# Performance work log

Measured on AMD Instinct MI355X. Metric: run time of the kernel, lower is better.

## Reference

```python
import jax, jax.numpy as jnp
import numpy as np

B, L, D = 2, 2048, 1024
H = 16
C = 128            # chunk_size
N = L // C         # num chunks
SCALE = float(np.sqrt(D))  # softmax_scale = sqrt(d_model)


def setup_inputs() -> dict:
    key = jax.random.key(0)
    ks = jax.random.split(key, 5)
    return {
        "x": jax.random.normal(ks[0], (B, L, D), dtype=jnp.float32),
        "w_qkv": jax.random.normal(ks[1], (D, 3 * D), dtype=jnp.float32) * (1.0 / np.sqrt(D)),
        "b_qkv": jax.random.normal(ks[2], (3 * D,), dtype=jnp.float32) * 0.02,
        "w_o": jax.random.normal(ks[3], (D, D), dtype=jnp.float32) * (1.0 / np.sqrt(D)),
        "b_o": jax.random.normal(ks[4], (D,), dtype=jnp.float32) * 0.02,
    }


def reference(x, w_qkv, b_qkv, w_o, b_o):
    b, l, d = x.shape
    hd = d // H
    qkv = x @ w_qkv + b_qkv                         # (B,L,3D)
    q, k, v = jnp.split(qkv, 3, axis=-1)
    q = q.reshape(b, l, H, hd)
    k = k.reshape(b, l, H, hd)
    v = v.reshape(b, l, H, hd)

    q_chunks = q.reshape(b, N, C, H, hd)
    k_chunks = k.reshape(b, N, C, H, hd)
    # mean_pool over the chunk dim
    q_pool = q_chunks.mean(axis=2)                  # (B,N,H,hd)
    k_pool = k_chunks.mean(axis=2)

    token2chunk = jnp.einsum('blhd,bnhd->bhln', q, k_pool)          # (B,H,L,N)
    chunk2token = jnp.einsum('bnhd,bnchd->bhnc', q_pool, k_chunks)  # (B,H,N,C)
    # outer product over (n,c) -> full (B,H,L,L) score matrix
    A = token2chunk[..., :, None] * chunk2token[:, :, None, :, :]   # (B,H,L,N,C)
    A = A.reshape(b, H, l, l)

    # direct intra-chunk attention overwrites the diagonal blocks
    direct = jnp.einsum('bnqhd,bnkhd->bhnqk', q_chunks, k_chunks)   # (B,H,N,C,C)
    A6 = A.reshape(b, H, N, C, N, C)
    eye = jnp.eye(N, dtype=bool)[:, None, :, None]                  # (N,1,N,1)
    A6 = jnp.where(eye, direct[:, :, :, :, None, :], A6)
    A = A6.reshape(b, H, l, l)

    # causal mask applied multiplicatively (masked scores become 0, NOT -inf)
    causal = jnp.tril(jnp.ones((l, l), dtype=bool))
    A = jnp.where(causal, A, 0.0) / SCALE
    A = jax.nn.softmax(A, axis=-1)

    out = jnp.einsum('bhqv,bvhd->bhqd', A, v)       # (B,H,L,hd)
    out = out.transpose(0, 2, 1, 3).reshape(b, l, d)
    return out @ w_o + b_o
```

## Files before the change

kernel.cpp:

```cpp
#include <hip/hip_runtime.h>
#include <math.h>

#define B_   2
#define L_   2048
#define D_   1024
#define H_   16
#define HD_  64
#define C_   128
#define N_   16
#define INV_SCALE 0.03125f

typedef _Float16 h8 __attribute__((ext_vector_type(8)));
typedef _Float16 h4 __attribute__((ext_vector_type(4)));
typedef float    f4 __attribute__((ext_vector_type(4)));

#define MFMA16(a, b, c) __builtin_amdgcn_mfma_f32_16x16x32_f16((a), (b), (c), 0, 0, 0)

__device__ __forceinline__ void gl_lds16(const void* g, void* l) {
  __builtin_amdgcn_global_load_lds(
      (const __attribute__((address_space(1))) void*)g,
      (__attribute__((address_space(3))) void*)l, 16, 0, 0);
}

__global__ __launch_bounds__(256) void prep_kernel(
    const float* __restrict__ X, _Float16* __restrict__ Xh,
    const float* __restrict__ Wq, _Float16* __restrict__ WqT,
    const float* __restrict__ Wo, _Float16* __restrict__ WoT)
{
  __shared__ float ts[32][36];
  const int tid = threadIdx.x;
  const int id = blockIdx.x;
  if (id < 4096) {
    int i = id * 1024 + tid * 4;
    float4 v = *(const float4*)(X + i);
    h4 o = { (_Float16)v.x, (_Float16)v.y, (_Float16)v.z, (_Float16)v.w };
    *(h4*)(Xh + i) = o;
    return;
  }
  const float* W; _Float16* WT; int Nc, bx, by;
  if (id < 7168) {
    int idx = id - 4096;
    W = Wq; WT = WqT; Nc = 3072; bx = idx % 96; by = idx / 96;
  } else {
    int idx = id - 7168;
    W = Wo; WT = WoT; Nc = 1024; bx = idx & 31; by = idx >> 5;
  }
  const int n0 = bx * 32, k0 = by * 32;
  {
    int kr = tid >> 3, nc4 = (tid & 7) * 4;
    float4 v = *(const float4*)&W[(size_t)(k0 + kr) * Nc + n0 + nc4];
    ts[kr][nc4+0] = v.x; ts[kr][nc4+1] = v.y; ts[kr][nc4+2] = v.z; ts[kr][nc4+3] = v.w;
  }
  __syncthreads();
  {
    int nr = tid >> 3, kc4 = (tid & 7) * 4;
    h4 o = { (_Float16)ts[kc4+0][nr], (_Float16)ts[kc4+1][nr],
             (_Float16)ts[kc4+2][nr], (_Float16)ts[kc4+3][nr] };
    *(h4*)&WT[(size_t)(n0 + nr) * 1024 + k0 + kc4] = o;
  }
}

template<int MT>
__global__ __launch_bounds__(256, 4) void gemm16_kernel(
    const _Float16* __restrict__ A, const _Float16* __restrict__ Bt,
    const float* __restrict__ bias,
    _Float16* __restrict__ Qh, _Float16* __restrict__ Kh, _Float16* __restrict__ VT,
    float* __restrict__ out,
    float* __restrict__ QP, float* __restrict__ KP, float* __restrict__ VCS,
    int Kd, int mode)
{
  constexpr int SM = MT / 32;
  __shared__ __align__(16) _Float16 As[2][MT * 32];
  __shared__ __align__(16) _Float16 Bs[2][4096];
  __shared__ float cred[2][128];
  const int tid = threadIdx.x;
  const int lane = tid & 63, w = tid >> 6;
  const int q = lane >> 4, r = lane & 15;
  const int mb = (w >> 1) * (MT / 2);
  const int nb = (w & 1) * 64;

  int m0, n0;
  {
    const int id = blockIdx.x;
    const int xcd = id & 7, slot = id >> 3;
    if constexpr (MT == 128) {
      n0 = (xcd * 3 + (slot % 3)) * 128;
      m0 = (slot / 3) * 128;
    } else {
      n0 = xcd * 128;
      m0 = slot * 64;
    }
  }

  const int Rr = tid >> 2;
  const int cd = (tid & 3) ^ ((Rr >> 1) & 3);
  const _Float16* Ag = A + (size_t)(m0 + Rr) * Kd + cd * 8;
  const _Float16* Bg = Bt + (size_t)(n0 + Rr) * Kd + cd * 8;
  const size_t rowStep = (size_t)64 * Kd;

  f4 acc[SM][4];
  #pragma unroll
  for (int s = 0; s < SM; ++s)
    #pragma unroll
    for (int t = 0; t < 4; ++t) acc[s][t] = (f4){0.f, 0.f, 0.f, 0.f};

  const int nIter = Kd >> 5;
  const int koff = (q ^ ((r >> 1) & 3)) << 3;

  auto stage = [&](int bf, int kt) {
    _Float16* Asl = &As[bf][w * 512];
    _Float16* Bsl = &Bs[bf][w * 512];
    gl_lds16(Ag + kt, Asl);
    if constexpr (MT == 128) gl_lds16(Ag + kt + rowStep, Asl + 2048);
    gl_lds16(Bg + kt, Bsl);
    gl_lds16(Bg + kt + rowStep, Bsl + 2048);
  };

  stage(0, 0);

  for (int it = 0; it < nIter; ++it) {
    __syncthreads();
    if (it + 1 < nIter) stage((it + 1) & 1, (it + 1) << 5);
    const _Float16* Ab = As[it & 1];
    const _Float16* Bb = Bs[it & 1];
    h8 af[SM], bf4[4];
    #pragma unroll
    for (int s = 0; s < SM; ++s)
      af[s] = *(const h8*)&Ab[(mb + s * 16 + r) * 32 + koff];
    #pragma unroll
    for (int t = 0; t < 4; ++t)
      bf4[t] = *(const h8*)&Bb[(nb + t * 16 + r) * 32 + koff];
    #pragma unroll
    for (int s = 0; s < SM; ++s)
      #pragma unroll
      for (int t = 0; t < 4; ++t)
        acc[s][t] = MFMA16(af[s], bf4[t], acc[s][t]);
  }

  if (mode == 0) {
    #pragma unroll
    for (int t = 0; t < 4; ++t) {
      int gn = n0 + nb + t * 16 + r;
      float bj = bias[gn];
      int which = gn >> 10, rem = gn & 1023;
      int h2 = rem >> 6, d2 = rem & 63;
      if (which < 2) {
        _Float16* dst = which == 0 ? Qh : Kh;
        #pragma unroll
        for (int s = 0; s < SM; ++s)
          #pragma unroll
          for (int i = 0; i < 4; ++i) {
            int gm = m0 + mb + s * 16 + q * 4 + i;
            int b2 = gm >> 11, l2 = gm & 2047;
            dst[(((size_t)(b2 * H_ + h2)) * L_ + l2) * HD_ + d2] =
                (_Float16)(acc[s][t][i] + bj);
          }
      } else {
        #pragma unroll
        for (int s = 0; s < SM; ++s) {
          int gm0 = m0 + mb + s * 16 + q * 4;
          int b2 = gm0 >> 11, l2 = gm0 & 2047;
          h4 hv = { (_Float16)(acc[s][t][0] + bj), (_Float16)(acc[s][t][1] + bj),
                    (_Float16)(acc[s][t][2] + bj), (_Float16)(acc[s][t][3] + bj) };
          *(h4*)&VT[((size_t)(b2 * H_ + h2) * HD_ + d2) * L_ + l2] = hv;
        }
      }
    }
    float colsum[4];
    #pragma unroll
    for (int t = 0; t < 4; ++t) {
      float s2 = 0.f;
      #pragma unroll
      for (int s = 0; s < SM; ++s)
        #pragma unroll
        for (int i = 0; i < 4; ++i) s2 += acc[s][t][i];
      s2 += __shfl_xor(s2, 16);
      s2 += __shfl_xor(s2, 32);
      colsum[t] = s2;
    }
    if (q == 0) {
      #pragma unroll
      for (int t = 0; t < 4; ++t)
        cred[w >> 1][nb + t * 16 + r] = colsum[t];
    }
    __syncthreads();
    if (tid < 128) {
      int jj = tid;
      float ssum = cred[0][jj] + cred[1][jj];
      int gn = n0 + jj;
      float bj = bias[gn];
      int which = gn >> 10, rem = gn & 1023;
      int h2 = rem >> 6, d2 = rem & 63;
      int b2 = m0 >> 11, nch = (m0 & 2047) >> 7;
      size_t o = (((size_t)(b2 * H_ + h2)) * N_ + nch) * HD_ + d2;
      if (which == 0)      QP[o] = ssum * (1.f / 128.f) + bj;
      else if (which == 1) KP[o] = ssum * (1.f / 128.f) + bj;
      else                 VCS[o] = ssum + 128.f * bj;
    }
  } else {
    #pragma unroll
    for (int t = 0; t < 4; ++t) {
      int gn = n0 + nb + t * 16 + r;
      float bj = bias[gn];
      #pragma unroll
      for (int s = 0; s < SM; ++s)
        #pragma unroll
        for (int i = 0; i < 4; ++i) {
          int gm = m0 + mb + s * 16 + q * 4 + i;
          out[(size_t)gm * 1024 + gn] = acc[s][t][i] + bj;
        }
    }
  }
}

__global__ __launch_bounds__(128) void pool2_kernel(
    const float* __restrict__ QP, const _Float16* __restrict__ Kh,
    const float* __restrict__ VCS,
    float* __restrict__ C2T, float* __restrict__ C2TMX, float* __restrict__ C2TMN,
    float* __restrict__ CSUF)
{
  __shared__ float qp_s[64];
  __shared__ float red[4];
  if (blockIdx.x >= 512) {
    int bh = blockIdx.x - 512, d = threadIdx.x;
    if (d < 64) {
      float run = 0.f;
      for (int n = N_ - 1; n >= 0; --n) {
        size_t o = ((size_t)bh * N_ + n) * HD_ + d;
        CSUF[o] = run;
        run += VCS[o];
      }
    }
    return;
  }
  int bh = blockIdx.x >> 4, n = blockIdx.x & 15, tid = threadIdx.x;
  int w = tid >> 6, lane = tid & 63;
  if (tid < 64) qp_s[tid] = QP[((size_t)bh * N_ + n) * HD_ + tid];
  const _Float16* kr = Kh + (((size_t)bh * L_) + n * C_ + tid) * HD_;
  h8 kv[8];
  #pragma unroll
  for (int c8 = 0; c8 < 8; ++c8) kv[c8] = *(const h8*)(kr + c8 * 8);
  __syncthreads();
  float s = 0.f;
  #pragma unroll
  for (int c8 = 0; c8 < 8; ++c8)
    #pragma unroll
    for (int j = 0; j < 8; ++j)
      s = fmaf((float)kv[c8][j], qp_s[c8 * 8 + j], s);
  C2T[((size_t)bh * N_ + n) * C_ + tid] = s;
  float mx = s, mn = s;
  #pragma unroll
  for (int st = 1; st <= 32; st <<= 1) {
    mx = fmaxf(mx, __shfl_xor(mx, st));
    mn = fminf(mn, __shfl_xor(mn, st));
  }
  if (lane == 0) { red[w * 2] = mx; red[w * 2 + 1] = mn; }
  __syncthreads();
  if (tid == 0) {
    C2TMX[bh * N_ + n] = fmaxf(red[0], red[2]);
    C2TMN[bh * N_ + n] = fminf(red[1], red[3]);
  }
}

__global__ __launch_bounds__(512, 4) void attn4_kernel(
    const _Float16* __restrict__ Qh, const _Float16* __restrict__ Kh,
    const _Float16* __restrict__ VT,
    const float* __restrict__ C2T, const float* __restrict__ C2TMX,
    const float* __restrict__ C2TMN, const float* __restrict__ CSUF,
    const float* __restrict__ KP, _Float16* __restrict__ AOh)
{
  __shared__ __align__(16) _Float16 buf0[8192];
  __shared__ __align__(16) _Float16 buf1[8192];
  __shared__ __align__(16) _Float16 buf2[8192];
  __shared__ __align__(16) _Float16 kp_s[1024];
  __shared__ __align__(16) float c2t_s[2][128];

  const int tid = threadIdx.x;
  const int w = tid >> 6, lane = tid & 63;
  const int q = lane >> 4, r = lane & 15;
  const int r7 = r & 7;
  const int id = blockIdx.x;
  const int bh = ((id & 7) << 2) + ((id >> 3) & 3);
  const int nq = 15 - (id >> 5);
  const int l0 = nq * 128;
  const int rowA = l0 + w * 16 + r;
  const int pcw = w * 16 + r;
  const size_t bhL = (size_t)bh * L_;
  const int b2 = bh >> 4, h2 = bh & 15;

  auto stageV = [&](_Float16* buf, int n) {
    #pragma unroll
    for (int j2 = 0; j2 < 2; ++j2) {
      int f = j2 * 512 + tid;
      int d = f >> 4, p = f & 15;
      int c16 = p ^ (d & 7);
      gl_lds16(VT + ((size_t)bh * HD_ + d) * L_ + n * C_ + c16 * 8,
               buf + (size_t)(j2 * 512 + w * 64) * 8);
    }
  };
  auto stageK = [&](_Float16* buf, int n) {
    #pragma unroll
    for (int j2 = 0; j2 < 2; ++j2) {
      int f = j2 * 512 + tid;
      int c = f >> 3, p = f & 7;
      int ck = p ^ (c & 7);
      gl_lds16(Kh + (bhL + n * C_ + c) * HD_ + ck * 8,
               buf + (size_t)(j2 * 512 + w * 64) * 8);
    }
  };
  auto stageC = [&](int bf, int n) {
    if (tid < 32)
      gl_lds16(C2T + ((size_t)bh * N_ + n) * C_ + tid * 4, &c2t_s[bf][0]);
  };

  if (tid < 256) {
    int n4 = tid >> 4, d4 = (tid & 15) * 4;
    float4 kpv = *(const float4*)&KP[((size_t)bh * N_ + n4) * HD_ + d4];
    int sd = ((((d4 >> 3) ^ (n4 & 7)) << 3) | (d4 & 7));
    h4 hv = { (_Float16)kpv.x, (_Float16)kpv.y, (_Float16)kpv.z, (_Float16)kpv.w };
    *(h4*)&kp_s[n4 * 64 + sd] = hv;
  }
  h8 qa0 = *(const h8*)(Qh + (bhL + rowA) * HD_ + q * 8);
  h8 qa1 = *(const h8*)(Qh + (bhL + rowA) * HD_ + 32 + q * 8);
  float mxL = C2TMX[bh * N_ + r];
  float mnL = C2TMN[bh * N_ + r];
  stageK(buf0, nq);
  stageV(buf2, nq);
  if (nq >= 1) stageC(0, nq - 1);
  __syncthreads();

  f4 tvacc = (f4){0.f, 0.f, 0.f, 0.f};
  {
    h8 kpa0 = *(const h8*)&kp_s[r * 64 + ((q ^ r7) << 3)];
    h8 kpa1 = *(const h8*)&kp_s[r * 64 + (((4 + q) ^ r7) << 3)];
    tvacc = MFMA16(kpa0, qa0, tvacc);
    tvacc = MFMA16(kpa1, qa1, tvacc);
  }
  float tvs[4];
  #pragma unroll
  for (int i = 0; i < 4; ++i) tvs[i] = tvacc[i] * INV_SCALE;

  float pm = -1e30f;
  #pragma unroll
  for (int i = 0; i < 4; ++i) {
    int n = q * 4 + i;
    float mx = __shfl(mxL, n);
    float mn = __shfl(mnL, n);
    float cm = fmaxf(tvs[i] * mx, tvs[i] * mn);
    pm = (n < nq) ? fmaxf(pm, cm) : pm;
  }
  pm = fmaxf(pm, __shfl_xor(pm, 16));
  pm = fmaxf(pm, __shfl_xor(pm, 32));

  f4 sc[8];
  #pragma unroll
  for (int u = 0; u < 8; ++u) sc[u] = (f4){0.f, 0.f, 0.f, 0.f};
  #pragma unroll
  for (int u = 0; u < 8; ++u) {
    h8 kb0 = *(const h8*)&buf0[(u * 16 + r) * 64 + ((q ^ r7) << 3)];
    h8 kb1 = *(const h8*)&buf0[(u * 16 + r) * 64 + (((4 + q) ^ r7) << 3)];
    sc[u] = MFMA16(qa0, kb0, sc[u]);
    sc[u] = MFMA16(qa1, kb1, sc[u]);
  }

  float rm[4] = {-1e30f, -1e30f, -1e30f, -1e30f};
  #pragma unroll
  for (int u = 0; u < 8; ++u) {
    int lcol = u * 16 + r;
    #pragma unroll
    for (int i = 0; i < 4; ++i) {
      int lrow = w * 16 + q * 4 + i;
      float v = sc[u][i] * INV_SCALE;
      v = (lcol <= lrow) ? v : -1e30f;
      sc[u][i] = v;
      rm[i] = fmaxf(rm[i], v);
    }
  }
  #pragma unroll
  for (int i = 0; i < 4; ++i) {
    rm[i] = fmaxf(rm[i], __shfl_xor(rm[i], 1));
    rm[i] = fmaxf(rm[i], __shfl_xor(rm[i], 2));
    rm[i] = fmaxf(rm[i], __shfl_xor(rm[i], 4));
    rm[i] = fmaxf(rm[i], __shfl_xor(rm[i], 8));
  }
  const int srcl = (r >> 2) << 4;
  const int ri = r & 3;
  float t0 = __shfl(rm[0], srcl), t1 = __shfl(rm[1], srcl);
  float t2 = __shfl(rm[2], srcl), t3 = __shfl(rm[3], srcl);
  float myrm = ri == 0 ? t0 : ri == 1 ? t1 : ri == 2 ? t2 : t3;

  const float M = fmaxf(fmaxf(pm, myrm), 0.f);
  const float e0 = __expf(-M);
  float Mc[4];
  #pragma unroll
  for (int i = 0; i < 4; ++i) Mc[i] = __shfl(M, (q << 2) + i);

  float cs[4] = {0.f, 0.f, 0.f, 0.f};
  #pragma unroll
  for (int u = 0; u < 8; ++u)
    #pragma unroll
    for (int i = 0; i < 4; ++i) {
      float v = sc[u][i];
      float p = (v > -1e29f) ? __expf(v - Mc[i]) : 0.f;
      sc[u][i] = p;
      cs[i] += p;
    }
  #pragma unroll
  for (int i = 0; i < 4; ++i) {
    cs[i] += __shfl_xor(cs[i], 1);
    cs[i] += __shfl_xor(cs[i], 2);
    cs[i] += __shfl_xor(cs[i], 4);
    cs[i] += __shfl_xor(cs[i], 8);
  }
  float c0 = __shfl(cs[0], srcl), c1 = __shfl(cs[1], srcl);
  float c2 = __shfl(cs[2], srcl), c3 = __shfl(cs[3], srcl);
  float den = ri == 0 ? c0 : ri == 1 ? c1 : ri == 2 ? c2 : c3;

  __syncthreads();

  _Float16* pw = (w < 4) ? (buf0 + w * 2048) : (buf1 + (w - 4) * 2048);
  #pragma unroll
  for (int u = 0; u < 8; ++u)
    #pragma unroll
    for (int i = 0; i < 4; ++i) {
      int row = q * 4 + i, col = u * 16 + r;
      pw[row * 128 + ((((col >> 3) ^ (row & 7)) << 3) | (col & 7))] =
          (_Float16)sc[u][i];
    }

  f4 oacc[4], sacc[4];
  #pragma unroll
  for (int t = 0; t < 4; ++t) {
    oacc[t] = (f4){0.f, 0.f, 0.f, 0.f};
    sacc[t] = (f4){0.f, 0.f, 0.f, 0.f};
  }
  #pragma unroll
  for (int s = 0; s < 4; ++s) {
    h8 pa = *(const h8*)&pw[r * 128 + (((s * 4 + q) ^ r7) << 3)];
    h8 mk;
    #pragma unroll
    for (int j2 = 0; j2 < 8; ++j2)
      mk[j2] = (_Float16)((s * 32 + q * 8 + j2 > pcw) ? 1.f : 0.f);
    #pragma unroll
    for (int t = 0; t < 4; ++t) {
      h8 vb = *(const h8*)&buf2[(t * 16 + r) * 128 + (((s * 4 + q) ^ r7) << 3)];
      oacc[t] = MFMA16(pa, vb, oacc[t]);
      sacc[t] = MFMA16(mk, vb, sacc[t]);
    }
  }

  __syncthreads();
  if (nq >= 1) stageV(buf1, nq - 1);

  for (int n = nq - 1; n >= 0; --n) {
    const int k = nq - 1 - n;
    _Float16* curb = (k & 1) ? buf2 : buf1;
    __syncthreads();
    if (n >= 1) {
      stageV((k & 1) ? buf1 : buf2, n - 1);
      stageC((k + 1) & 1, n - 1);
    }
    int i0 = n & 3;
    float tvx = i0 == 0 ? tvs[0] : i0 == 1 ? tvs[1] : i0 == 2 ? tvs[2] : tvs[3];
    float tvn = __shfl(tvx, ((n >> 2) << 4) + r);
    float csum = 0.f;
    const float* c2p = c2t_s[k & 1];
    #pragma unroll
    for (int s = 0; s < 4; ++s) {
      const float* cp = &c2p[s * 32 + q * 8];
      float4 ca = *(const float4*)cp;
      float4 cb = *(const float4*)(cp + 4);
      float p0 = __expf(tvn * ca.x - M), p1 = __expf(tvn * ca.y - M);
      float p2 = __expf(tvn * ca.z - M), p3 = __expf(tvn * ca.w - M);
      float p4 = __expf(tvn * cb.x - M), p5 = __expf(tvn * cb.y - M);
      float p6 = __expf(tvn * cb.z - M), p7 = __expf(tvn * cb.w - M);
      csum += p0 + p1 + p2 + p3 + p4 + p5 + p6 + p7;
      h8 pa = { (_Float16)p0, (_Float16)p1, (_Float16)p2, (_Float16)p3,
                (_Float16)p4, (_Float16)p5, (_Float16)p6, (_Float16)p7 };
      #pragma unroll
      for (int t = 0; t < 4; ++t) {
        h8 vb = *(const h8*)&curb[(t * 16 + r) * 128 + (((s * 4 + q) ^ r7) << 3)];
        oacc[t] = MFMA16(pa, vb, oacc[t]);
      }
    }
    csum += __shfl_xor(csum, 16);
    csum += __shfl_xor(csum, 32);
    den += csum;
  }

  int cnt = (L_ - 1) - rowA;
  den += e0 * (float)cnt;
  float e0r[4], dnr[4];
  #pragma unroll
  for (int i = 0; i < 4; ++i) {
    e0r[i] = __shfl(e0,  (q << 2) + i);
    dnr[i] = __shfl(den, (q << 2) + i);
  }
  #pragma unroll
  for (int t = 0; t < 4; ++t) {
    int d = t * 16 + r;
    float csf = CSUF[((size_t)bh * N_ + nq) * HD_ + d];
    #pragma unroll
    for (int i = 0; i < 4; ++i) {
      int row = l0 + w * 16 + q * 4 + i;
      float suffix = sacc[t][i] + csf;
      float o = (oacc[t][i] + e0r[i] * suffix) / dnr[i];
      AOh[((size_t)b2 * L_ + row) * D_ + h2 * HD_ + d] = (_Float16)o;
    }
  }
}

extern "C" void kernel_launch(void* const* d_in, const int* in_sizes, int n_in,
                              void* d_out, int out_size, void* d_ws, size_t ws_size,
                              hipStream_t stream)
{
  (void)in_sizes; (void)n_in; (void)out_size; (void)ws_size;
  const float* x     = (const float*)d_in[0];
  const float* w_qkv = (const float*)d_in[1];
  const float* b_qkv = (const float*)d_in[2];
  const float* w_o   = (const float*)d_in[3];
  const float* b_o   = (const float*)d_in[4];
  float* out = (float*)d_out;

  char* p = (char*)d_ws;
  _Float16* xh   = (_Float16*)p; p += (size_t)4194304 * 2;
  _Float16* wqT  = (_Float16*)p; p += (size_t)3145728 * 2;
  _Float16* woT  = (_Float16*)p; p += (size_t)1048576 * 2;
  _Float16* Qh   = (_Float16*)p; p += (size_t)4194304 * 2;
  _Float16* Kh   = (_Float16*)p; p += (size_t)4194304 * 2;
  _Float16* VT   = (_Float16*)p; p += (size_t)4194304 * 2;
  _Float16* AOh  = (_Float16*)p; p += (size_t)4194304 * 2;
  float*    C2T  = (float*)p;    p += (size_t)65536 * 4;
  float*    QP   = (float*)p;    p += (size_t)32768 * 4;
  float*    KP   = (float*)p;    p += (size_t)32768 * 4;
  float*    VCS  = (float*)p;    p += (size_t)32768 * 4;
  float*    CSUF = (float*)p;    p += (size_t)32768 * 4;
  float*    MXa  = (float*)p;    p += (size_t)512 * 4;
  float*    MNa  = (float*)p;    p += (size_t)512 * 4;

  prep_kernel<<<8192, 256, 0, stream>>>(x, xh, w_qkv, wqT, w_o, woT);
  gemm16_kernel<128><<<768, 256, 0, stream>>>(
      xh, wqT, b_qkv, Qh, Kh, VT, nullptr, QP, KP, VCS, D_, 0);
  pool2_kernel<<<544, 128, 0, stream>>>(QP, Kh, VCS, C2T, MXa, MNa, CSUF);
  attn4_kernel<<<512, 512, 0, stream>>>(
      Qh, Kh, VT, C2T, MXa, MNa, CSUF, KP, AOh);
  gemm16_kernel<64><<<512, 256, 0, stream>>>(
      AOh, woT, b_o, nullptr, nullptr, nullptr, out, nullptr, nullptr, nullptr, D_, 1);
}
```

Baseline: 179.5 us.

## Replace QKV GEMM with 256x256-tile pipelined kernel and remap output GEMM blocks

Adds a dedicated QKV projection kernel that uses 256x256 output tiles, 512 threads, double-buffered global-to-LDS loads and explicit waitcnt/sched barriers with setprio around MFMA bursts. It fuses the bias add, head scatter and chunk pooling epilogue the same way the generic kernel did. Larger tiles raise operand reuse and cut global traffic, but the grid shrinks to 192 blocks, fewer than the device's CU count, so some compute units sit idle. The output-projection GEMM also gets a new block-to-XCD mapping that groups M rows per XCD, aiming at better L2 locality.

```diff
diff --git a/kernel.cpp b/kernel.cpp
--- a/kernel.cpp
+++ b/kernel.cpp
@@ -21,6 +21,14 @@
       (const __attribute__((address_space(1))) void*)g,
       (__attribute__((address_space(3))) void*)l, 16, 0, 0);
 }
+
+#define SBAR()  do { __builtin_amdgcn_sched_barrier(0); \
+                     __builtin_amdgcn_s_barrier();      \
+                     __builtin_amdgcn_sched_barrier(0); } while (0)
+#define LGKM0() do { asm volatile("s_waitcnt lgkmcnt(0)" ::: "memory"); \
+                     __builtin_amdgcn_sched_barrier(0); } while (0)
+#define VMW(n)  do { asm volatile("s_waitcnt vmcnt(" #n ")" ::: "memory"); \
+                     __builtin_amdgcn_sched_barrier(0); } while (0)
 
 __global__ __launch_bounds__(256) void prep_kernel(
     const float* __restrict__ X, _Float16* __restrict__ Xh,
@@ -57,6 +65,172 @@
     h4 o = { (_Float16)ts[kc4+0][nr], (_Float16)ts[kc4+1][nr],
              (_Float16)ts[kc4+2][nr], (_Float16)ts[kc4+3][nr] };
     *(h4*)&WT[(size_t)(n0 + nr) * 1024 + k0 + kc4] = o;
+  }
+}
+
+__global__ __launch_bounds__(512, 2) void qkv256_kernel(
+    const _Float16* __restrict__ A, const _Float16* __restrict__ Bt,
+    const float* __restrict__ bias,
+    _Float16* __restrict__ Qh, _Float16* __restrict__ Kh, _Float16* __restrict__ VT,
+    float* __restrict__ QP, float* __restrict__ KP, float* __restrict__ VCS)
+{
+  __shared__ __align__(16) _Float16 As[2][16384];
+  __shared__ __align__(16) _Float16 Bs[2][16384];
+
+  const int tid = threadIdx.x;
+  const int w = tid >> 6, lane = tid & 63;
+  const int q = lane >> 4, r = lane & 15, r7 = r & 7;
+  const int wm = w >> 2, wn = w & 3;
+
+  const int id = blockIdx.x, xcd = id & 7, slot = id >> 3;
+  const int m0 = ((xcd >> 1) * 4 + (slot & 3)) * 256;
+  const int n0 = ((xcd & 1) * 6 + (slot >> 2)) * 256;
+
+  const int srow = tid >> 3;
+  const int spart = (tid & 7) ^ (srow & 7);
+  const _Float16* Asrc = A  + (size_t)(m0 + srow) * 1024 + spart * 8;
+  const _Float16* Bsrc = Bt + (size_t)(n0 + srow) * 1024 + spart * 8;
+  const int ldst = w * 512;
+
+  const int aoffb = (wm * 128 + r) * 64;
+  const int boffb = (wn * 64 + r) * 64;
+  const int k0s = (q ^ r7) << 3;
+  const int k1s = ((4 + q) ^ r7) << 3;
+
+  auto stA = [&](int cc, int ko, int qq) {
+    gl_lds16(Asrc + (size_t)qq * 65536 + ko, &As[cc][qq * 4096 + ldst]);
+  };
+  auto stB = [&](int cc, int ko, int qq) {
+    gl_lds16(Bsrc + (size_t)qq * 65536 + ko, &Bs[cc][qq * 4096 + ldst]);
+  };
+
+  f4 acc[8][4];
+  #pragma unroll
+  for (int m = 0; m < 8; ++m)
+    #pragma unroll
+    for (int n = 0; n < 4; ++n) acc[m][n] = (f4){0.f, 0.f, 0.f, 0.f};
+
+  stB(0, 0, 0); stB(0, 0, 1); stB(0, 0, 2); stB(0, 0, 3);
+  stA(0, 0, 0); stA(0, 0, 2); stA(0, 0, 1); stA(0, 0, 3);
+  VMW(2);
+  SBAR();
+
+  for (int t = 0; t < 16; ++t) {
+    const int c = t & 1;
+    const _Float16* __restrict__ Ab = As[c];
+    const _Float16* __restrict__ Bb = Bs[c];
+    const int kt = (t + 1) << 6;
+    const bool pf = (t < 15);
+    h8 af[4], bf[4];
+
+    #pragma unroll
+    for (int m = 0; m < 4; ++m) af[m] = *(const h8*)&Ab[aoffb + m * 1024 + k0s];
+    #pragma unroll
+    for (int n = 0; n < 4; ++n) bf[n] = *(const h8*)&Bb[boffb + n * 1024 + k0s];
+    if (pf) { stB(c ^ 1, kt, 0); stB(c ^ 1, kt, 1); }
+    SBAR();
+    LGKM0();
+    __builtin_amdgcn_s_setprio(1);
+    #pragma unroll
+    for (int m = 0; m < 4; ++m)
+      #pragma unroll
+      for (int n = 0; n < 4; ++n) acc[m][n] = MFMA16(af[m], bf[n], acc[m][n]);
+    __builtin_amdgcn_s_setprio(0);
+    __builtin_amdgcn_sched_barrier(0);
+    if (pf) { VMW(2); } else { VMW(0); }
+    SBAR();
+
+    #pragma unroll
+    for (int m = 0; m < 4; ++m) af[m] = *(const h8*)&Ab[aoffb + (4 + m) * 1024 + k0s];
+    if (pf) { stB(c ^ 1, kt, 2); stB(c ^ 1, kt, 3); }
+    SBAR();
+    LGKM0();
+    __builtin_amdgcn_s_setprio(1);
+    #pragma unroll
+    for (int m = 0; m < 4; ++m)
+      #pragma unroll
+      for (int n = 0; n < 4; ++n) acc[4 + m][n] = MFMA16(af[m], bf[n], acc[4 + m][n]);
+    __builtin_amdgcn_s_setprio(0);
+    __builtin_amdgcn_sched_barrier(0);
+    SBAR();
+
+    #pragma unroll
+    for (int m = 0; m < 4; ++m) af[m] = *(const h8*)&Ab[aoffb + m * 1024 + k1s];
+    #pragma unroll
+    for (int n = 0; n < 4; ++n) bf[n] = *(const h8*)&Bb[boffb + n * 1024 + k1s];
+    if (pf) { stA(c ^ 1, kt, 0); stA(c ^ 1, kt, 2); }
+    SBAR();
+    LGKM0();
+    __builtin_amdgcn_s_setprio(1);
+    #pragma unroll
+    for (int m = 0; m < 4; ++m)
+      #pragma unroll
+      for (int n = 0; n < 4; ++n) acc[m][n] = MFMA16(af[m], bf[n], acc[m][n]);
+    __builtin_amdgcn_s_setprio(0);
+    __builtin_amdgcn_sched_barrier(0);
+    SBAR();
+
+    #pragma unroll
+    for (int m = 0; m < 4; ++m) af[m] = *(const h8*)&Ab[aoffb + (4 + m) * 1024 + k1s];
+    if (pf) {
+      stA(c ^ 1, kt, 1); stA(c ^ 1, kt, 3);
+      VMW(2);
+    }
+    SBAR();
+    LGKM0();
+    __builtin_amdgcn_s_setprio(1);
+    #pragma unroll
+    for (int m = 0; m < 4; ++m)
+      #pragma unroll
+      for (int n = 0; n < 4; ++n) acc[4 + m][n] = MFMA16(af[m], bf[n], acc[4 + m][n]);
+    __builtin_amdgcn_s_setprio(0);
+    __builtin_amdgcn_sched_barrier(0);
+    SBAR();
+  }
+
+  const int rb = m0 + wm * 128;
+  const int b2 = rb >> 11;
+  const int nch = (rb & 2047) >> 7;
+  #pragma unroll
+  for (int tc = 0; tc < 4; ++tc) {
+    const int gn = n0 + wn * 64 + tc * 16 + r;
+    const float bj = bias[gn];
+    const int which = gn >> 10, rem = gn & 1023;
+    const int h2 = rem >> 6, d2 = rem & 63;
+    if (which < 2) {
+      _Float16* dst = which == 0 ? Qh : Kh;
+      #pragma unroll
+      for (int m = 0; m < 8; ++m)
+        #pragma unroll
+        for (int i = 0; i < 4; ++i) {
+          const int gm = rb + m * 16 + q * 4 + i;
+          const int l2 = gm & 2047;
+          dst[(((size_t)(b2 * H_ + h2)) * L_ + l2) * HD_ + d2] =
+              (_Float16)(acc[m][tc][i] + bj);
+        }
+    } else {
+      #pragma unroll
+      for (int m = 0; m < 8; ++m) {
+        const int gm0 = rb + m * 16 + q * 4;
+        const int l2 = gm0 & 2047;
+        h4 hv = { (_Float16)(acc[m][tc][0] + bj), (_Float16)(acc[m][tc][1] + bj),
+                  (_Float16)(acc[m][tc][2] + bj), (_Float16)(acc[m][tc][3] + bj) };
+        *(h4*)&VT[((size_t)(b2 * H_ + h2) * HD_ + d2) * L_ + l2] = hv;
+      }
+    }
+    float s2 = 0.f;
+    #pragma unroll
+    for (int m = 0; m < 8; ++m)
+      #pragma unroll
+      for (int i = 0; i < 4; ++i) s2 += acc[m][tc][i];
+    s2 += __shfl_xor(s2, 16);
+    s2 += __shfl_xor(s2, 32);
+    if (q == 0) {
+      const size_t o = (((size_t)(b2 * H_ + h2)) * N_ + nch) * HD_ + d2;
+      if (which == 0)      QP[o] = s2 * (1.f / 128.f) + bj;
+      else if (which == 1) KP[o] = s2 * (1.f / 128.f) + bj;
+      else                 VCS[o] = s2 + 128.f * bj;
+    }
   }
 }
 
@@ -87,8 +261,8 @@
       n0 = (xcd * 3 + (slot % 3)) * 128;
       m0 = (slot / 3) * 128;
     } else {
-      n0 = xcd * 128;
-      m0 = slot * 64;
+      m0 = (xcd * 8 + (slot >> 3)) * 64;
+      n0 = (slot & 7) * 128;
     }
   }
 
@@ -539,8 +713,8 @@
   float*    MNa  = (float*)p;    p += (size_t)512 * 4;
 
   prep_kernel<<<8192, 256, 0, stream>>>(x, xh, w_qkv, wqT, w_o, woT);
-  gemm16_kernel<128><<<768, 256, 0, stream>>>(
-      xh, wqT, b_qkv, Qh, Kh, VT, nullptr, QP, KP, VCS, D_, 0);
+  qkv256_kernel<<<192, 512, 0, stream>>>(
+      xh, wqT, b_qkv, Qh, Kh, VT, QP, KP, VCS);
   pool2_kernel<<<544, 128, 0, stream>>>(QP, Kh, VCS, C2T, MXa, MNa, CSUF);
   attn4_kernel<<<512, 512, 0, stream>>>(
       Qh, Kh, VT, C2T, MXa, MNa, CSUF, KP, AOh);
```

Result: no change. 179.5 us (+0.0%).
